# Performance work log

Measured on AMD Instinct MI355X. Metric: run time of the kernel, lower is better.

The kernel has to match this reference:

```python
import jax, jax.numpy as jnp
import numpy as np

N = 100000      # nodes
E = 1600000     # edges (before self loops)
F_IN = 128      # num_graph_features
H = 2           # heads
C = 64          # out channels per head (output // 2)
G = 64          # graphs in batch
NEG_SLOPE = 0.2


def setup_inputs() -> dict:
    key = jax.random.key(0)
    ks = jax.random.split(key, 11)
    s = 0.1  # weight scale to keep activations well-conditioned
    return {
        "x": jax.random.normal(ks[0], (N, F_IN), jnp.float32),
        "edge_index": jax.random.randint(ks[1], (2, E), 0, N, jnp.int32),
        "batch": jnp.sort(jax.random.randint(ks[2], (N,), 0, G, jnp.int32)),
        "W1": jax.random.normal(ks[3], (F_IN, H * C), jnp.float32) * s,
        "a1_src": jax.random.normal(ks[4], (H, C), jnp.float32) * s,
        "a1_dst": jax.random.normal(ks[5], (H, C), jnp.float32) * s,
        "b1": jnp.zeros((H * C,), jnp.float32),
        "W2": jax.random.normal(ks[6], (H * C, H * C), jnp.float32) * s,
        "a2_src": jax.random.normal(ks[7], (H, C), jnp.float32) * s,
        "a2_dst": jax.random.normal(ks[8], (H, C), jnp.float32) * s,
        "b2": jnp.zeros((H * C,), jnp.float32),
    }


def gat_conv(x, src, dst, W, a_src, a_dst, bias, n):
    # PyG GATConv (shared lin, concat=True): h: [n, H, C]
    h = (x @ W).reshape(n, H, C)
    alpha_src = jnp.sum(h * a_src, axis=-1)          # [n, H]
    alpha_dst = jnp.sum(h * a_dst, axis=-1)          # [n, H]
    e = jax.nn.leaky_relu(alpha_src[src] + alpha_dst[dst], NEG_SLOPE)  # [E', H]
    # segment softmax over edges grouped by destination node
    m = jax.ops.segment_max(e, dst, num_segments=n)  # [n, H]
    ex = jnp.exp(e - m[dst])
    denom = jax.ops.segment_sum(ex, dst, num_segments=n)
    alpha = ex / (denom[dst] + 1e-16)                # [E', H]
    out = jax.ops.segment_sum(alpha[:, :, None] * h[src], dst, num_segments=n)
    return out.reshape(n, H * C) + bias


def reference(x, edge_index, batch, W1, a1_src, a1_dst, b1, W2, a2_src, a2_dst, b2):
    # edge/node masks assumed all-valid (identity filtering)
    loops = jnp.arange(N, dtype=edge_index.dtype)    # add_self_loops=True
    src = jnp.concatenate([edge_index[0], loops])
    dst = jnp.concatenate([edge_index[1], loops])
    h1 = jax.nn.relu(gat_conv(x, src, dst, W1, a1_src, a1_dst, b1, N))
    h2 = gat_conv(h1, src, dst, W2, a2_src, a2_dst, b2, N)
    # global_mean_pool over batch ids
    pooled = jax.ops.segment_sum(h2, batch, num_segments=G)
    counts = jax.ops.segment_sum(jnp.ones((N,), h2.dtype), batch, num_segments=G)
    return pooled / jnp.maximum(counts, 1.0)[:, None]
```

## Files before the change

### kernel.cpp

```cpp
#include <hip/hip_runtime.h>

#define N_NODES 100000
#define N_EDGES 1600000
#define F_IN    128
#define HC      128
#define NGRAPH  64
#define NEG_SLOPE 0.2f

static constexpr int TOT_E = N_EDGES + N_NODES;

#define CHUNK  2048
#define NBLK   831
#define NBUCK  196

typedef __bf16 bf16x8 __attribute__((ext_vector_type(8)));
typedef float  f32x4  __attribute__((ext_vector_type(4)));

__device__ __forceinline__ unsigned short f2bf_rne(float f) {
    unsigned u = __float_as_uint(f);
    u += 0x7fffu + ((u >> 16) & 1u);
    return (unsigned short)(u >> 16);
}
__device__ __forceinline__ float bf2f(unsigned b) {
    return __uint_as_float(b << 16);
}


__global__ __launch_bounds__(256) void binpart_kernel(const int* __restrict__ ei,
                                                      unsigned* __restrict__ pairs,
                                                      int* __restrict__ seg_start,
                                                      int* __restrict__ seg_cnt) {
    __shared__ int cnt[256];
    __shared__ int wtot[4];
    int t = threadIdx.x, blk = blockIdx.x;
    int lane = t & 63, w = t >> 6;
    long base = (long)blk * CHUNK;

    cnt[t] = 0;
    __syncthreads();

    for (int j = t; j < CHUNK; j += 256) {
        long i = base + j;
        int d = -1;
        if (i < N_EDGES)    d = ei[N_EDGES + i];
        else if (i < TOT_E) d = (int)(i - N_EDGES);
        if (d >= 0) atomicAdd(&cnt[d >> 9], 1);
    }
    __syncthreads();

    int c = cnt[t];
    int x = c;
#pragma unroll
    for (int off = 1; off < 64; off <<= 1) {
        int v = __shfl_up(x, off);
        if (lane >= off) x += v;
    }
    if (lane == 63) wtot[w] = x;
    __syncthreads();
    int add = 0;
#pragma unroll
    for (int k = 0; k < 3; ++k) if (k < w) add += wtot[k];
    x += add;
    int st = x - c;
    if (t < NBUCK) {
        seg_start[(size_t)blk * NBUCK + t] = st;
        seg_cnt[(size_t)blk * NBUCK + t]   = c;
    }
    __syncthreads();
    cnt[t] = st;
    __syncthreads();

    for (int j = t; j < CHUNK; j += 256) {
        long i = base + j;
        int s = -1, d = -1;
        if (i < N_EDGES)    { s = ei[i]; d = ei[N_EDGES + i]; }
        else if (i < TOT_E) { s = (int)(i - N_EDGES); d = s; }
        if (d >= 0) {
            int pos = atomicAdd(&cnt[d >> 9], 1);
            pairs[base + pos] = ((unsigned)s << 9) | ((unsigned)d & 511u);
        }
    }
}


__global__ __launch_bounds__(256) void btot_kernel(const int* __restrict__ seg_cnt, int* __restrict__ btot) {
    int b = blockIdx.x, t = threadIdx.x;
    int s = 0;
    for (int j = t; j < NBLK; j += 256) s += seg_cnt[(size_t)j * NBUCK + b];
    for (int off = 32; off; off >>= 1) s += __shfl_down(s, off);
    __shared__ int ws[4];
    int lane = t & 63, w = t >> 6;
    if (lane == 0) ws[w] = s;
    __syncthreads();
    if (t == 0) btot[b] = ws[0] + ws[1] + ws[2] + ws[3];
}

__global__ __launch_bounds__(256) void bbase_kernel(const int* __restrict__ btot, int* __restrict__ bbase) {
    int t = threadIdx.x;
    int lane = t & 63, w = t >> 6;
    int v = (t < NBUCK) ? btot[t] : 0;
    int x = v;
#pragma unroll
    for (int off = 1; off < 64; off <<= 1) {
        int u = __shfl_up(x, off);
        if (lane >= off) x += u;
    }
    __shared__ int wt[4];
    if (lane == 63) wt[w] = x;
    __syncthreads();
    int add = 0;
#pragma unroll
    for (int k = 0; k < 3; ++k) if (k < w) add += wt[k];
    x += add;
    if (t < NBUCK) bbase[t] = x - v;
}


__global__ __launch_bounds__(1024) void bucket_build(const unsigned* __restrict__ pairs,
                                                     const int* __restrict__ seg_start,
                                                     const int* __restrict__ seg_cnt,
                                                     const int* __restrict__ bbase,
                                                     int* __restrict__ offs,
                                                     int* __restrict__ csr_src) {
    int b = blockIdx.x, t = threadIdx.x;
    int nodeBase = b << 9;
    __shared__ int cur[512];
    __shared__ int pref[NBLK];
    __shared__ int sstart[NBLK];
    __shared__ int wt2[16];

    if (t < 512) cur[t] = 0;
    for (int j = t; j < NBLK; j += 1024) {
        pref[j]   = seg_cnt[(size_t)j * NBUCK + b];
        sstart[j] = seg_start[(size_t)j * NBUCK + b];
    }
    __syncthreads();
    for (int off = 1; off < NBLK; off <<= 1) {
        int v = 0;
        if (t < NBLK && t >= off) v = pref[t - off];
        __syncthreads();
        if (t < NBLK) pref[t] += v;
        __syncthreads();
    }
    int M = pref[NBLK - 1];

    for (int j = t; j < M; j += 1024) {
        int lo = 0, hi = NBLK - 1;
        while (lo < hi) { int mid = (lo + hi) >> 1; if (pref[mid] > j) hi = mid; else lo = mid + 1; }
        int within = j - (lo ? pref[lo - 1] : 0);
        unsigned wd = pairs[(size_t)lo * CHUNK + sstart[lo] + within];
        atomicAdd(&cur[wd & 511u], 1);
    }
    __syncthreads();

    int lane = t & 63, w = t >> 6;
    int myc = (t < 512) ? cur[t] : 0;
    int x = myc;
#pragma unroll
    for (int off = 1; off < 64; off <<= 1) {
        int u = __shfl_up(x, off);
        if (lane >= off) x += u;
    }
    if (lane == 63) wt2[w] = x;
    __syncthreads();
    int add = 0;
#pragma unroll
    for (int k = 0; k < 15; ++k) if (k < w) add += wt2[k];
    x += add;
    int gstart = bbase[b] + x - myc;
    if (t < 512) {
        if (nodeBase + t <= N_NODES) offs[nodeBase + t] = gstart;
        cur[t] = gstart;
    }
    __syncthreads();

    for (int j = t; j < M; j += 1024) {
        int lo = 0, hi = NBLK - 1;
        while (lo < hi) { int mid = (lo + hi) >> 1; if (pref[mid] > j) hi = mid; else lo = mid + 1; }
        int within = j - (lo ? pref[lo - 1] : 0);
        unsigned wd = pairs[(size_t)lo * CHUNK + sstart[lo] + within];
        int pos = atomicAdd(&cur[wd & 511u], 1);
        csr_src[pos] = (int)(wd >> 9);
    }
}

__global__ __launch_bounds__(256) void counts_kernel(const int* __restrict__ batch, int* __restrict__ counts) {
    __shared__ int loc[NGRAPH];
    int t = threadIdx.x;
    if (t < NGRAPH) loc[t] = 0;
    __syncthreads();
    int i = blockIdx.x * 256 + t;
    if (i < N_NODES) atomicAdd(&loc[batch[i]], 1);
    __syncthreads();
    if (t < NGRAPH && loc[t]) atomicAdd(&counts[t], loc[t]);
}


__global__ __launch_bounds__(256) void wtconv_kernel(const float* __restrict__ W, unsigned short* __restrict__ Wt) {
    int i = blockIdx.x * 256 + threadIdx.x;
    if (i >= F_IN * HC) return;
    int k = i >> 7, col = i & 127;
    Wt[(size_t)(k >> 3) * (HC * 8) + col * 8 + (k & 7)] = f2bf_rne(W[i]);
}


template<bool BF16IN>
__global__ __launch_bounds__(256) void gemm_mfma(const void* __restrict__ Xv,
                                                 const unsigned short* __restrict__ Wt,
                                                 unsigned short* __restrict__ Hout,
                                                 const float* __restrict__ a_src,
                                                 const float* __restrict__ a_dst,
                                                 float* __restrict__ asrc,
                                                 float* __restrict__ adst) {
    __shared__ unsigned short A_lds[64 * F_IN];
    int t = threadIdx.x;
    int lane = t & 63, wave = t >> 6;
    int wc = wave & 1, wr = wave >> 1;
    int base = blockIdx.x * 64;

    bf16x8 Bf[4][4];
    {
        int colb = wc * 64 + (lane & 15);
        int kbb  = lane >> 4;
#pragma unroll
        for (int ct = 0; ct < 4; ++ct)
#pragma unroll
            for (int ks = 0; ks < 4; ++ks) {
                int kb = kbb + 4 * ks;
                Bf[ct][ks] = *(const bf16x8*)&Wt[(size_t)kb * (HC * 8) + (colb + ct * 16) * 8];
            }
    }

#pragma unroll
    for (int it = 0; it < 8; ++it) {
        int i = t + it * 256;
        int row = i >> 5, c4 = i & 31, k0 = c4 * 4;
        uint2 pk; pk.x = 0; pk.y = 0;
        if (base + row < N_NODES) {
            if (BF16IN) {
                pk = ((const uint2*)Xv)[(size_t)(base + row) * 32 + c4];
            } else {
                float4 v = ((const float4*)Xv)[(size_t)(base + row) * 32 + c4];
                pk.x = (unsigned)f2bf_rne(v.x) | ((unsigned)f2bf_rne(v.y) << 16);
                pk.y = (unsigned)f2bf_rne(v.z) | ((unsigned)f2bf_rne(v.w) << 16);
            }
        }
        int byte = row * 256 + (((k0 >> 3) ^ (row & 7)) << 4) + (k0 & 4) * 2;
        *(uint2*)((char*)A_lds + byte) = pk;
    }
    __syncthreads();

    f32x4 acc[2][4] = {};
#pragma unroll
    for (int ks = 0; ks < 4; ++ks) {
        bf16x8 Af[2];
#pragma unroll
        for (int r = 0; r < 2; ++r) {
            int row = wr * 32 + r * 16 + (lane & 15);
            int kb  = ks * 4 + (lane >> 4);
            int byte = row * 256 + ((kb ^ (row & 7)) << 4);
            Af[r] = *(const bf16x8*)((const char*)A_lds + byte);
        }
#pragma unroll
        for (int ct = 0; ct < 4; ++ct) {
            acc[0][ct] = __builtin_amdgcn_mfma_f32_16x16x32_bf16(Af[0], Bf[ct][ks], acc[0][ct], 0, 0, 0);
            acc[1][ct] = __builtin_amdgcn_mfma_f32_16x16x32_bf16(Af[1], Bf[ct][ks], acc[1][ct], 0, 0, 0);
        }
    }

#pragma unroll
    for (int r = 0; r < 2; ++r) {
        int row0 = base + wr * 32 + r * 16 + (lane >> 4) * 4;
#pragma unroll
        for (int reg = 0; reg < 4; ++reg) {
            int row = row0 + reg;
            if (row < N_NODES) {
#pragma unroll
                for (int ct = 0; ct < 4; ++ct) {
                    int col = wc * 64 + ct * 16 + (lane & 15);
                    Hout[(size_t)row * HC + col] = f2bf_rne(acc[r][ct][reg]);
                }
            }
        }
    }

    float as_c[4], ad_c[4];
#pragma unroll
    for (int ct = 0; ct < 4; ++ct) {
        int ch = wc * 64 + ct * 16 + (lane & 15);
        as_c[ct] = a_src[ch];
        ad_c[ct] = a_dst[ch];
    }
#pragma unroll
    for (int r = 0; r < 2; ++r) {
#pragma unroll
        for (int reg = 0; reg < 4; ++reg) {
            float ps = acc[r][0][reg] * as_c[0] + acc[r][1][reg] * as_c[1]
                     + acc[r][2][reg] * as_c[2] + acc[r][3][reg] * as_c[3];
            float pd = acc[r][0][reg] * ad_c[0] + acc[r][1][reg] * ad_c[1]
                     + acc[r][2][reg] * ad_c[2] + acc[r][3][reg] * ad_c[3];
#pragma unroll
            for (int off = 1; off < 16; off <<= 1) {
                ps += __shfl_xor(ps, off);
                pd += __shfl_xor(pd, off);
            }
            if ((lane & 15) == 0) {
                int row = base + wr * 32 + r * 16 + (lane >> 4) * 4 + reg;
                if (row < N_NODES) {
                    asrc[(size_t)row * 2 + wc] = ps;
                    adst[(size_t)row * 2 + wc] = pd;
                }
            }
        }
    }
}


__global__ __launch_bounds__(256) void agg_kernel(const int* __restrict__ offs, const int* __restrict__ csr_src,
                                                  const float* __restrict__ asrc, const float* __restrict__ adst,
                                                  const unsigned short* __restrict__ Hin,
                                                  const float* __restrict__ bias,
                                                  unsigned short* __restrict__ Hout, int do_relu) {
    int wid  = (blockIdx.x * 256 + threadIdx.x) >> 6;
    int lane = threadIdx.x & 63;
    if (wid >= N_NODES) return;
    int beg = offs[wid], end = offs[wid + 1];
    int grp   = lane >> 3;
    int head  = grp & 1;
    int eslot = grp >> 1;
    int q8    = lane & 7;
    float2 adv = *(const float2*)&adst[(size_t)wid * 2];
    float madst = head ? adv.y : adv.x;
    const float2* av = (const float2*)asrc;
    const unsigned short* hbase = Hin + head * 64 + q8 * 8;

    float den = 0.f;
    float a0c = 0.f, a1c = 0.f, a2c = 0.f, a3c = 0.f;
    float a4c = 0.f, a5c = 0.f, a6c = 0.f, a7c = 0.f;

    for (int e = beg + eslot; e < end; e += 8) {
        int en = e + 4;
        bool v1 = en < end;
        int s0 = csr_src[e];
        int s1 = v1 ? csr_src[en] : s0;
        float2 aa0 = av[s0];
        float2 aa1 = av[s1];
        uint4 g0 = *(const uint4*)&hbase[(size_t)s0 * HC];
        uint4 g1 = *(const uint4*)&hbase[(size_t)s1 * HC];
        float l0 = (head ? aa0.y : aa0.x) + madst; l0 = l0 > 0.f ? l0 : NEG_SLOPE * l0;
        float l1 = (head ? aa1.y : aa1.x) + madst; l1 = l1 > 0.f ? l1 : NEG_SLOPE * l1;
        float w0 = __expf(l0);
        float w1 = v1 ? __expf(l1) : 0.f;
        den += w0 + w1;
        a0c = fmaf(w1, bf2f(g1.x & 0xffffu), fmaf(w0, bf2f(g0.x & 0xffffu), a0c));
        a1c = fmaf(w1, bf2f(g1.x >> 16),     fmaf(w0, bf2f(g0.x >> 16),     a1c));
        a2c = fmaf(w1, bf2f(g1.y & 0xffffu), fmaf(w0, bf2f(g0.y & 0xffffu), a2c));
        a3c = fmaf(w1, bf2f(g1.y >> 16),     fmaf(w0, bf2f(g0.y >> 16),     a3c));
        a4c = fmaf(w1, bf2f(g1.z & 0xffffu), fmaf(w0, bf2f(g0.z & 0xffffu), a4c));
        a5c = fmaf(w1, bf2f(g1.z >> 16),     fmaf(w0, bf2f(g0.z >> 16),     a5c));
        a6c = fmaf(w1, bf2f(g1.w & 0xffffu), fmaf(w0, bf2f(g0.w & 0xffffu), a6c));
        a7c = fmaf(w1, bf2f(g1.w >> 16),     fmaf(w0, bf2f(g0.w >> 16),     a7c));
    }

#pragma unroll
    for (int off = 16; off <= 32; off <<= 1) {
        den += __shfl_xor(den, off);
        a0c += __shfl_xor(a0c, off);
        a1c += __shfl_xor(a1c, off);
        a2c += __shfl_xor(a2c, off);
        a3c += __shfl_xor(a3c, off);
        a4c += __shfl_xor(a4c, off);
        a5c += __shfl_xor(a5c, off);
        a6c += __shfl_xor(a6c, off);
        a7c += __shfl_xor(a7c, off);
    }

    if (lane < 16) {
        float inv = 1.0f / den;
        float4 b0 = *(const float4*)&bias[lane * 8];
        float4 b1 = *(const float4*)&bias[lane * 8 + 4];
        float o0 = fmaf(a0c, inv, b0.x);
        float o1 = fmaf(a1c, inv, b0.y);
        float o2 = fmaf(a2c, inv, b0.z);
        float o3 = fmaf(a3c, inv, b0.w);
        float o4 = fmaf(a4c, inv, b1.x);
        float o5 = fmaf(a5c, inv, b1.y);
        float o6 = fmaf(a6c, inv, b1.z);
        float o7 = fmaf(a7c, inv, b1.w);
        if (do_relu) {
            o0 = fmaxf(o0, 0.f); o1 = fmaxf(o1, 0.f); o2 = fmaxf(o2, 0.f); o3 = fmaxf(o3, 0.f);
            o4 = fmaxf(o4, 0.f); o5 = fmaxf(o5, 0.f); o6 = fmaxf(o6, 0.f); o7 = fmaxf(o7, 0.f);
        }
        uint4 st;
        st.x = (unsigned)f2bf_rne(o0) | ((unsigned)f2bf_rne(o1) << 16);
        st.y = (unsigned)f2bf_rne(o2) | ((unsigned)f2bf_rne(o3) << 16);
        st.z = (unsigned)f2bf_rne(o4) | ((unsigned)f2bf_rne(o5) << 16);
        st.w = (unsigned)f2bf_rne(o6) | ((unsigned)f2bf_rne(o7) << 16);
        *(uint4*)&Hout[(size_t)wid * HC + lane * 8] = st;
    }
}


__global__ __launch_bounds__(256) void pool_kernel(const unsigned short* __restrict__ H2,
                                                   const int* __restrict__ counts,
                                                   float* __restrict__ out) {
    int g = blockIdx.x;
    int chunk = blockIdx.y;
    __shared__ int soff, scnt;
    if (threadIdx.x == 0) {
        int s = 0;
        for (int i = 0; i < g; ++i) s += counts[i];
        soff = s; scnt = counts[g];
    }
    __syncthreads();
    int start = soff, cnt = scnt;
    int r = threadIdx.x >> 7;
    int c = threadIdx.x & 127;
    float acc = 0.f;
    for (int v = chunk * 2 + r; v < cnt; v += 16)
        acc += bf2f((unsigned)H2[(size_t)(start + v) * HC + c]);
    float inv = 1.0f / fmaxf((float)cnt, 1.0f);
    atomicAdd(&out[g * HC + c], acc * inv);
}


extern "C" void kernel_launch(void* const* d_in, const int* in_sizes, int n_in,
                              void* d_out, int out_size, void* d_ws, size_t ws_size,
                              hipStream_t stream) {
    const float* x     = (const float*)d_in[0];
    const int*   ei    = (const int*)d_in[1];
    const int*   batch = (const int*)d_in[2];
    const float* W1    = (const float*)d_in[3];
    const float* a1s   = (const float*)d_in[4];
    const float* a1d   = (const float*)d_in[5];
    const float* b1    = (const float*)d_in[6];
    const float* W2    = (const float*)d_in[7];
    const float* a2s   = (const float*)d_in[8];
    const float* a2d   = (const float*)d_in[9];
    const float* b2    = (const float*)d_in[10];
    float* out = (float*)d_out;

    char* ws = (char*)d_ws;
    const size_t NH = (size_t)N_NODES * HC;
    unsigned short* hA = (unsigned short*)ws;
    unsigned short* hB = hA + NH;
    unsigned* pairs = (unsigned*)(hB + NH);
    float* asrc = (float*)(pairs + (size_t)NBLK * CHUNK);
    float* adst = asrc + (size_t)N_NODES * 2;
    unsigned short* wt1 = (unsigned short*)(adst + (size_t)N_NODES * 2);
    unsigned short* wt2 = wt1 + F_IN * HC;
    int*   offs = (int*)(wt2 + F_IN * HC);
    int*   csr  = offs + (N_NODES + 1);
    int*   seg_start = csr + TOT_E;
    int*   seg_cnt   = seg_start + (size_t)NBLK * NBUCK;
    int*   btot = seg_cnt + (size_t)NBLK * NBUCK;
    int*   bbase = btot + NBUCK;
    int*   counts = bbase + NBUCK;

    hipMemsetAsync(counts, 0, NGRAPH * sizeof(int), stream);
    hipMemsetAsync(out, 0, (size_t)out_size * sizeof(float), stream);

    wtconv_kernel<<<(F_IN * HC + 255) / 256, 256, 0, stream>>>(W1, wt1);
    wtconv_kernel<<<(F_IN * HC + 255) / 256, 256, 0, stream>>>(W2, wt2);
    counts_kernel<<<(N_NODES + 255) / 256, 256, 0, stream>>>(batch, counts);

    binpart_kernel<<<NBLK, 256, 0, stream>>>(ei, pairs, seg_start, seg_cnt);
    btot_kernel<<<NBUCK, 256, 0, stream>>>(seg_cnt, btot);
    bbase_kernel<<<1, 256, 0, stream>>>(btot, bbase);
    bucket_build<<<NBUCK, 1024, 0, stream>>>(pairs, seg_start, seg_cnt, bbase, offs, csr);

    int gemmBlocks = (N_NODES + 63) / 64;
    int waveBlocks = (N_NODES + 3) / 4;

    gemm_mfma<false><<<gemmBlocks, 256, 0, stream>>>(x, wt1, hA, a1s, a1d, asrc, adst);
    agg_kernel<<<waveBlocks, 256, 0, stream>>>(offs, csr, asrc, adst, hA, b1, hB, 1);

    gemm_mfma<true><<<gemmBlocks, 256, 0, stream>>>(hB, wt2, hA, a2s, a2d, asrc, adst);
    agg_kernel<<<waveBlocks, 256, 0, stream>>>(offs, csr, asrc, adst, hA, b2, hB, 0);

    pool_kernel<<<dim3(NGRAPH, 8), 256, 0, stream>>>(hB, counts, out);
}
```

Measured before the change: 281.2 us.

## Fuse layer-1 GEMM, edge binning and graph counts into one heterogeneous launch

```diff
diff --git a/kernel.cpp b/kernel.cpp
--- a/kernel.cpp
+++ b/kernel.cpp
@@ -13,6 +13,9 @@
 #define NBLK   831
 #define NBUCK  196
 
+#define GEMM_B 1563
+#define CNT_B  391
+
 typedef __bf16 bf16x8 __attribute__((ext_vector_type(8)));
 typedef float  f32x4  __attribute__((ext_vector_type(4)));
 
@@ -26,13 +29,12 @@
 }
 
 
-__global__ __launch_bounds__(256) void binpart_kernel(const int* __restrict__ ei,
-                                                      unsigned* __restrict__ pairs,
-                                                      int* __restrict__ seg_start,
-                                                      int* __restrict__ seg_cnt) {
-    __shared__ int cnt[256];
-    __shared__ int wtot[4];
-    int t = threadIdx.x, blk = blockIdx.x;
+__device__ __forceinline__ void binpart_body(int blk, int t,
+                                             const int* __restrict__ ei,
+                                             unsigned* __restrict__ pairs,
+                                             int* __restrict__ seg_start,
+                                             int* __restrict__ seg_cnt,
+                                             int* cnt, int* wtot) {
     int lane = t & 63, w = t >> 6;
     long base = (long)blk * CHUNK;
 
@@ -80,6 +82,165 @@
             pairs[base + pos] = ((unsigned)s << 9) | ((unsigned)d & 511u);
         }
     }
+}
+
+template<bool BF16IN>
+__device__ __forceinline__ void gemm_body(int gbid, int t,
+                                          const void* __restrict__ Xv,
+                                          const unsigned short* __restrict__ Wt,
+                                          unsigned short* __restrict__ Hout,
+                                          const float* __restrict__ a_src,
+                                          const float* __restrict__ a_dst,
+                                          float* __restrict__ asrc,
+                                          float* __restrict__ adst,
+                                          unsigned short* A_lds) {
+    int lane = t & 63, wave = t >> 6;
+    int wc = wave & 1, wr = wave >> 1;
+    int base = gbid * 64;
+
+    bf16x8 Bf[4][4];
+    {
+        int colb = wc * 64 + (lane & 15);
+        int kbb  = lane >> 4;
+#pragma unroll
+        for (int ct = 0; ct < 4; ++ct)
+#pragma unroll
+            for (int ks = 0; ks < 4; ++ks) {
+                int kb = kbb + 4 * ks;
+                Bf[ct][ks] = *(const bf16x8*)&Wt[(size_t)kb * (HC * 8) + (colb + ct * 16) * 8];
+            }
+    }
+
+#pragma unroll
+    for (int it = 0; it < 8; ++it) {
+        int i = t + it * 256;
+        int row = i >> 5, c4 = i & 31, k0 = c4 * 4;
+        uint2 pk; pk.x = 0; pk.y = 0;
+        if (base + row < N_NODES) {
+            if (BF16IN) {
+                pk = ((const uint2*)Xv)[(size_t)(base + row) * 32 + c4];
+            } else {
+                float4 v = ((const float4*)Xv)[(size_t)(base + row) * 32 + c4];
+                pk.x = (unsigned)f2bf_rne(v.x) | ((unsigned)f2bf_rne(v.y) << 16);
+                pk.y = (unsigned)f2bf_rne(v.z) | ((unsigned)f2bf_rne(v.w) << 16);
+            }
+        }
+        int byte = row * 256 + (((k0 >> 3) ^ (row & 7)) << 4) + (k0 & 4) * 2;
+        *(uint2*)((char*)A_lds + byte) = pk;
+    }
+    __syncthreads();
+
+    f32x4 acc[2][4] = {};
+#pragma unroll
+    for (int ks = 0; ks < 4; ++ks) {
+        bf16x8 Af[2];
+#pragma unroll
+        for (int r = 0; r < 2; ++r) {
+            int row = wr * 32 + r * 16 + (lane & 15);
+            int kb  = ks * 4 + (lane >> 4);
+            int byte = row * 256 + ((kb ^ (row & 7)) << 4);
+            Af[r] = *(const bf16x8*)((const char*)A_lds + byte);
+        }
+#pragma unroll
+        for (int ct = 0; ct < 4; ++ct) {
+            acc[0][ct] = __builtin_amdgcn_mfma_f32_16x16x32_bf16(Af[0], Bf[ct][ks], acc[0][ct], 0, 0, 0);
+            acc[1][ct] = __builtin_amdgcn_mfma_f32_16x16x32_bf16(Af[1], Bf[ct][ks], acc[1][ct], 0, 0, 0);
+        }
+    }
+
+#pragma unroll
+    for (int r = 0; r < 2; ++r) {
+        int row0 = base + wr * 32 + r * 16 + (lane >> 4) * 4;
+#pragma unroll
+        for (int reg = 0; reg < 4; ++reg) {
+            int row = row0 + reg;
+            if (row < N_NODES) {
+#pragma unroll
+                for (int ct = 0; ct < 4; ++ct) {
+                    int col = wc * 64 + ct * 16 + (lane & 15);
+                    Hout[(size_t)row * HC + col] = f2bf_rne(acc[r][ct][reg]);
+                }
+            }
+        }
+    }
+
+    float as_c[4], ad_c[4];
+#pragma unroll
+    for (int ct = 0; ct < 4; ++ct) {
+        int ch = wc * 64 + ct * 16 + (lane & 15);
+        as_c[ct] = a_src[ch];
+        ad_c[ct] = a_dst[ch];
+    }
+#pragma unroll
+    for (int r = 0; r < 2; ++r) {
+#pragma unroll
+        for (int reg = 0; reg < 4; ++reg) {
+            float ps = acc[r][0][reg] * as_c[0] + acc[r][1][reg] * as_c[1]
+                     + acc[r][2][reg] * as_c[2] + acc[r][3][reg] * as_c[3];
+            float pd = acc[r][0][reg] * ad_c[0] + acc[r][1][reg] * ad_c[1]
+                     + acc[r][2][reg] * ad_c[2] + acc[r][3][reg] * ad_c[3];
+#pragma unroll
+            for (int off = 1; off < 16; off <<= 1) {
+                ps += __shfl_xor(ps, off);
+                pd += __shfl_xor(pd, off);
+            }
+            if ((lane & 15) == 0) {
+                int row = base + wr * 32 + r * 16 + (lane >> 4) * 4 + reg;
+                if (row < N_NODES) {
+                    asrc[(size_t)row * 2 + wc] = ps;
+                    adst[(size_t)row * 2 + wc] = pd;
+                }
+            }
+        }
+    }
+}
+
+
+__global__ __launch_bounds__(256) void fused_main(const float* __restrict__ x,
+                                                  const unsigned short* __restrict__ wt1,
+                                                  unsigned short* __restrict__ hA,
+                                                  const float* __restrict__ a1s,
+                                                  const float* __restrict__ a1d,
+                                                  float* __restrict__ asrc,
+                                                  float* __restrict__ adst,
+                                                  const int* __restrict__ ei,
+                                                  unsigned* __restrict__ pairs,
+                                                  int* __restrict__ seg_start,
+                                                  int* __restrict__ seg_cnt,
+                                                  const int* __restrict__ batch,
+                                                  int* __restrict__ counts) {
+    __shared__ unsigned short A_lds[64 * F_IN];
+    __shared__ int cnt[256];
+    __shared__ int wtot[4];
+    __shared__ int loc[NGRAPH];
+    int bid = blockIdx.x, t = threadIdx.x;
+
+    if (bid < 2 * NBLK) {
+        if (bid & 1) binpart_body(bid >> 1, t, ei, pairs, seg_start, seg_cnt, cnt, wtot);
+        else         gemm_body<false>(bid >> 1, t, x, wt1, hA, a1s, a1d, asrc, adst, A_lds);
+    } else if (bid < NBLK + GEMM_B) {
+        gemm_body<false>(bid - NBLK, t, x, wt1, hA, a1s, a1d, asrc, adst, A_lds);
+    } else {
+        int cb = bid - (NBLK + GEMM_B);
+        if (t < NGRAPH) loc[t] = 0;
+        __syncthreads();
+        int i = cb * 256 + t;
+        if (i < N_NODES) atomicAdd(&loc[batch[i]], 1);
+        __syncthreads();
+        if (t < NGRAPH && loc[t]) atomicAdd(&counts[t], loc[t]);
+    }
+}
+
+
+__global__ __launch_bounds__(256) void gemm2_kernel(const unsigned short* __restrict__ Xv,
+                                                    const unsigned short* __restrict__ Wt,
+                                                    unsigned short* __restrict__ Hout,
+                                                    const float* __restrict__ a_src,
+                                                    const float* __restrict__ a_dst,
+                                                    float* __restrict__ asrc,
+                                                    float* __restrict__ adst) {
+    __shared__ unsigned short A_lds[64 * F_IN];
+    gemm_body<true>(blockIdx.x, threadIdx.x, Xv, Wt, Hout, a_src, a_dst, asrc, adst, A_lds);
 }
 
 
@@ -184,134 +345,16 @@
     }
 }
 
-__global__ __launch_bounds__(256) void counts_kernel(const int* __restrict__ batch, int* __restrict__ counts) {
-    __shared__ int loc[NGRAPH];
-    int t = threadIdx.x;
-    if (t < NGRAPH) loc[t] = 0;
-    __syncthreads();
-    int i = blockIdx.x * 256 + t;
-    if (i < N_NODES) atomicAdd(&loc[batch[i]], 1);
-    __syncthreads();
-    if (t < NGRAPH && loc[t]) atomicAdd(&counts[t], loc[t]);
-}
-
-
-__global__ __launch_bounds__(256) void wtconv_kernel(const float* __restrict__ W, unsigned short* __restrict__ Wt) {
+
+__global__ __launch_bounds__(256) void wtconv_both(const float* __restrict__ W1, const float* __restrict__ W2,
+                                                   unsigned short* __restrict__ Wt1, unsigned short* __restrict__ Wt2) {
     int i = blockIdx.x * 256 + threadIdx.x;
-    if (i >= F_IN * HC) return;
-    int k = i >> 7, col = i & 127;
-    Wt[(size_t)(k >> 3) * (HC * 8) + col * 8 + (k & 7)] = f2bf_rne(W[i]);
-}
-
-
-template<bool BF16IN>
-__global__ __launch_bounds__(256) void gemm_mfma(const void* __restrict__ Xv,
-                                                 const unsigned short* __restrict__ Wt,
-                                                 unsigned short* __restrict__ Hout,
-                                                 const float* __restrict__ a_src,
-                                                 const float* __restrict__ a_dst,
-                                                 float* __restrict__ asrc,
-                                                 float* __restrict__ adst) {
-    __shared__ unsigned short A_lds[64 * F_IN];
-    int t = threadIdx.x;
-    int lane = t & 63, wave = t >> 6;
-    int wc = wave & 1, wr = wave >> 1;
-    int base = blockIdx.x * 64;
-
-    bf16x8 Bf[4][4];
-    {
-        int colb = wc * 64 + (lane & 15);
-        int kbb  = lane >> 4;
-#pragma unroll
-        for (int ct = 0; ct < 4; ++ct)
-#pragma unroll
-            for (int ks = 0; ks < 4; ++ks) {
-                int kb = kbb + 4 * ks;
-                Bf[ct][ks] = *(const bf16x8*)&Wt[(size_t)kb * (HC * 8) + (colb + ct * 16) * 8];
-            }
-    }
-
-#pragma unroll
-    for (int it = 0; it < 8; ++it) {
-        int i = t + it * 256;
-        int row = i >> 5, c4 = i & 31, k0 = c4 * 4;
-        uint2 pk; pk.x = 0; pk.y = 0;
-        if (base + row < N_NODES) {
-            if (BF16IN) {
-                pk = ((const uint2*)Xv)[(size_t)(base + row) * 32 + c4];
-            } else {
-                float4 v = ((const float4*)Xv)[(size_t)(base + row) * 32 + c4];
-                pk.x = (unsigned)f2bf_rne(v.x) | ((unsigned)f2bf_rne(v.y) << 16);
-                pk.y = (unsigned)f2bf_rne(v.z) | ((unsigned)f2bf_rne(v.w) << 16);
-            }
-        }
-        int byte = row * 256 + (((k0 >> 3) ^ (row & 7)) << 4) + (k0 & 4) * 2;
-        *(uint2*)((char*)A_lds + byte) = pk;
-    }
-    __syncthreads();
-
-    f32x4 acc[2][4] = {};
-#pragma unroll
-    for (int ks = 0; ks < 4; ++ks) {
-        bf16x8 Af[2];
-#pragma unroll
-        for (int r = 0; r < 2; ++r) {
-            int row = wr * 32 + r * 16 + (lane & 15);
-            int kb  = ks * 4 + (lane >> 4);
-            int byte = row * 256 + ((kb ^ (row & 7)) << 4);
-            Af[r] = *(const bf16x8*)((const char*)A_lds + byte);
-        }
-#pragma unroll
-        for (int ct = 0; ct < 4; ++ct) {
-            acc[0][ct] = __builtin_amdgcn_mfma_f32_16x16x32_bf16(Af[0], Bf[ct][ks], acc[0][ct], 0, 0, 0);
-            acc[1][ct] = __builtin_amdgcn_mfma_f32_16x16x32_bf16(Af[1], Bf[ct][ks], acc[1][ct], 0, 0, 0);
-        }
-    }
-
-#pragma unroll
-    for (int r = 0; r < 2; ++r) {
-        int row0 = base + wr * 32 + r * 16 + (lane >> 4) * 4;
-#pragma unroll
-        for (int reg = 0; reg < 4; ++reg) {
-            int row = row0 + reg;
-            if (row < N_NODES) {
-#pragma unroll
-                for (int ct = 0; ct < 4; ++ct) {
-                    int col = wc * 64 + ct * 16 + (lane & 15);
-                    Hout[(size_t)row * HC + col] = f2bf_rne(acc[r][ct][reg]);
-                }
-            }
-        }
-    }
-
-    float as_c[4], ad_c[4];
-#pragma unroll
-    for (int ct = 0; ct < 4; ++ct) {
-        int ch = wc * 64 + ct * 16 + (lane & 15);
-        as_c[ct] = a_src[ch];
-        ad_c[ct] = a_dst[ch];
-    }
-#pragma unroll
-    for (int r = 0; r < 2; ++r) {
-#pragma unroll
-        for (int reg = 0; reg < 4; ++reg) {
-            float ps = acc[r][0][reg] * as_c[0] + acc[r][1][reg] * as_c[1]
-                     + acc[r][2][reg] * as_c[2] + acc[r][3][reg] * as_c[3];
-            float pd = acc[r][0][reg] * ad_c[0] + acc[r][1][reg] * ad_c[1]
-                     + acc[r][2][reg] * ad_c[2] + acc[r][3][reg] * ad_c[3];
-#pragma unroll
-            for (int off = 1; off < 16; off <<= 1) {
-                ps += __shfl_xor(ps, off);
-                pd += __shfl_xor(pd, off);
-            }
-            if ((lane & 15) == 0) {
-                int row = base + wr * 32 + r * 16 + (lane >> 4) * 4 + reg;
-                if (row < N_NODES) {
-                    asrc[(size_t)row * 2 + wc] = ps;
-                    adst[(size_t)row * 2 + wc] = pd;
-                }
-            }
-        }
+    const float* W = (i < F_IN * HC) ? W1 : W2;
+    unsigned short* Wt = (i < F_IN * HC) ? Wt1 : Wt2;
+    int j = (i < F_IN * HC) ? i : i - F_IN * HC;
+    if (j < F_IN * HC) {
+        int k = j >> 7, col = j & 127;
+        Wt[(size_t)(k >> 3) * (HC * 8) + col * 8 + (k & 7)] = f2bf_rne(W[j]);
     }
 }
 
@@ -460,22 +503,21 @@
     hipMemsetAsync(counts, 0, NGRAPH * sizeof(int), stream);
     hipMemsetAsync(out, 0, (size_t)out_size * sizeof(float), stream);
 
-    wtconv_kernel<<<(F_IN * HC + 255) / 256, 256, 0, stream>>>(W1, wt1);
-    wtconv_kernel<<<(F_IN * HC + 255) / 256, 256, 0, stream>>>(W2, wt2);
-    counts_kernel<<<(N_NODES + 255) / 256, 256, 0, stream>>>(batch, counts);
-
-    binpart_kernel<<<NBLK, 256, 0, stream>>>(ei, pairs, seg_start, seg_cnt);
+    wtconv_both<<<(2 * F_IN * HC + 255) / 256, 256, 0, stream>>>(W1, W2, wt1, wt2);
+
+    fused_main<<<GEMM_B + NBLK + CNT_B, 256, 0, stream>>>(x, wt1, hA, a1s, a1d, asrc, adst,
+                                                          ei, pairs, seg_start, seg_cnt,
+                                                          batch, counts);
+
     btot_kernel<<<NBUCK, 256, 0, stream>>>(seg_cnt, btot);
     bbase_kernel<<<1, 256, 0, stream>>>(btot, bbase);
     bucket_build<<<NBUCK, 1024, 0, stream>>>(pairs, seg_start, seg_cnt, bbase, offs, csr);
 
-    int gemmBlocks = (N_NODES + 63) / 64;
     int waveBlocks = (N_NODES + 3) / 4;
 
-    gemm_mfma<false><<<gemmBlocks, 256, 0, stream>>>(x, wt1, hA, a1s, a1d, asrc, adst);
     agg_kernel<<<waveBlocks, 256, 0, stream>>>(offs, csr, asrc, adst, hA, b1, hB, 1);
 
-    gemm_mfma<true><<<gemmBlocks, 256, 0, stream>>>(hB, wt2, hA, a2s, a2d, asrc, adst);
+    gemm2_kernel<<<GEMM_B, 256, 0, stream>>>(hB, wt2, hA, a2s, a2d, asrc, adst);
     agg_kernel<<<waveBlocks, 256, 0, stream>>>(offs, csr, asrc, adst, hA, b2, hB, 0);
 
     pool_kernel<<<dim3(NGRAPH, 8), 256, 0, stream>>>(hB, counts, out);
```

After: 272.1 us. 1.03x faster.
